# Kernel optimization log

Hardware: AMD Instinct MI355X
Metric: run time of the kernel (lower is better)

Reference implementation:

```python
import jax, jax.numpy as jnp
import numpy as np

D_MODEL, D_K, D_V = 512, 64, 64


def setup_inputs() -> dict:
    key = jax.random.key(0)
    ks = jax.random.split(key, 9)
    b, n = 8, 4096
    scale = 1.0 / np.sqrt(D_MODEL)
    return {
        "q": jax.random.normal(ks[0], (b, n, D_MODEL), jnp.float32),
        "k": jax.random.normal(ks[1], (b, n, D_MODEL), jnp.float32),
        "v": jax.random.normal(ks[2], (b, n, D_MODEL), jnp.float32),
        "Wq": jax.random.normal(ks[3], (D_MODEL, D_K), jnp.float32) * scale,
        "bq": jnp.zeros((D_K,), jnp.float32),
        "Wk": jax.random.normal(ks[4], (D_MODEL, D_K), jnp.float32) * scale,
        "bk": jnp.zeros((D_K,), jnp.float32),
        "Wv": jax.random.normal(ks[5], (D_MODEL, D_V), jnp.float32) * scale,
        "bv": jnp.zeros((D_V,), jnp.float32),
        "mask": 0,
    }


def reference(q, k, v, Wq, bq, Wk, bk, Wv, bv, mask):
    # linear projections (torch Linear: x @ W^T + b; here W stored as [in,out])
    qp = jnp.einsum("bnd,de->bne", q, Wq) + bq  # (b,n,d_k)
    kp = jnp.einsum("bnd,de->bne", k, Wk) + bk  # (b,n,d_k)
    vp = jnp.einsum("bnd,de->bne", v, Wv) + bv  # (b,n,d_v)
    temper = D_K ** 0.5
    attn = jnp.einsum("bqe,bke->bqk", qp, kp) / temper  # (b,n,n)
    # original: attn[attn == mask] = -inf (equality mask on scores)
    attn = jnp.where(attn == jnp.float32(mask), -jnp.inf, attn)
    # NOTE: original's `attn.masked_fill(look_ahead_mask==0, -inf)` is NOT
    # in-place and its result is discarded, so look_ahead_mask has no effect.
    attn = jax.nn.softmax(attn, axis=-1)
    return jnp.einsum("bqk,bkv->bqv", attn, vp)  # (b,n,d_v)
```

## Files before the change

### kernel.cpp

```cpp
#include <hip/hip_runtime.h>

typedef _Float16 f16;
typedef _Float16 f16x2 __attribute__((ext_vector_type(2)));
typedef _Float16 f16x4 __attribute__((ext_vector_type(4)));
typedef _Float16 f16x8 __attribute__((ext_vector_type(8)));
typedef __fp16   h16x2 __attribute__((ext_vector_type(2)));
typedef float    f32x4 __attribute__((ext_vector_type(4)));
typedef float    f32x16 __attribute__((ext_vector_type(16)));

static constexpr float L2E = 1.44269504088896340736f;
static constexpr float QSC = 0.18033688011112042f;

static __device__ __forceinline__ f32x4 mfma16(f16x8 a, f16x8 b, f32x4 c) {
    return __builtin_amdgcn_mfma_f32_16x16x32_f16(a, b, c, 0, 0, 0);
}
static __device__ __forceinline__ f32x16 mfma32(f16x8 a, f16x8 b, f32x16 c) {
    return __builtin_amdgcn_mfma_f32_32x32x16_f16(a, b, c, 0, 0, 0);
}
static __device__ __forceinline__ f16x2 cvt_pk(float a, float b) {
    h16x2 t = __builtin_amdgcn_cvt_pkrtz(a, b);
    return __builtin_bit_cast(f16x2, t);
}
static __device__ __forceinline__ void gload16(const void* g, void* l) {
    __builtin_amdgcn_global_load_lds(
        (const __attribute__((address_space(1))) unsigned int*)g,
        (__attribute__((address_space(3))) unsigned int*)l, 16, 0, 0);
}

__global__ void ah_wt_prep(const float* __restrict__ Wq,
                           const float* __restrict__ Wk,
                           const float* __restrict__ Wv,
                           f16* __restrict__ WT) {
    const float* W = (blockIdx.x == 0) ? Wq : (blockIdx.x == 1) ? Wk : Wv;
    f16* o = WT + (size_t)blockIdx.x * (64 * 512);
    for (int i = threadIdx.x; i < 64 * 512; i += blockDim.x) {
        int col = i >> 9, e = i & 511;
        o[i] = (f16)W[e * 64 + col];
    }
}

__global__ __launch_bounds__(256) void ah_proj(
    const float* __restrict__ Xq, const float* __restrict__ Xk, const float* __restrict__ Xv,
    const float* __restrict__ bq, const float* __restrict__ bk, const float* __restrict__ bv,
    const f16* __restrict__ WT,
    f16* __restrict__ qp, f16* __restrict__ kp, f16* __restrict__ vpT) {

    const int tens = blockIdx.y;
    const float* X    = (tens == 0) ? Xq : (tens == 1) ? Xk : Xv;
    const float* bias = (tens == 0) ? bq : (tens == 1) ? bk : bv;
    const f16* wt = WT + (size_t)tens * (64 * 512);
    const float osc = (tens == 0) ? QSC : 1.0f;

    const int lane = threadIdx.x & 63;
    const int wave = threadIdx.x >> 6;
    const int l15 = lane & 15, g = lane >> 4;
    const int row0 = blockIdx.x * 128;
    const int wrow = wave * 32;

    f32x4 acc[2][4];
#pragma unroll
    for (int a = 0; a < 2; ++a)
#pragma unroll
        for (int b = 0; b < 4; ++b) acc[a][b] = (f32x4){0.f, 0.f, 0.f, 0.f};

#pragma unroll 4
    for (int ec = 0; ec < 16; ++ec) {
        f16x8 af[2];
#pragma unroll
        for (int rf = 0; rf < 2; ++rf) {
            const float* px = X + (size_t)(row0 + wrow + rf * 16 + l15) * 512 + ec * 32 + g * 8;
            float4 v0 = *(const float4*)px;
            float4 v1 = *(const float4*)(px + 4);
            f16x2 p0 = cvt_pk(v0.x, v0.y);
            f16x2 p1 = cvt_pk(v0.z, v0.w);
            f16x2 p2 = cvt_pk(v1.x, v1.y);
            f16x2 p3 = cvt_pk(v1.z, v1.w);
            f16x8 a;
            a[0] = p0[0]; a[1] = p0[1]; a[2] = p1[0]; a[3] = p1[1];
            a[4] = p2[0]; a[5] = p2[1]; a[6] = p3[0]; a[7] = p3[1];
            af[rf] = a;
        }
#pragma unroll
        for (int cf = 0; cf < 4; ++cf) {
            f16x8 bfr = *(const f16x8*)(wt + (size_t)(cf * 16 + l15) * 512 + ec * 32 + g * 8);
#pragma unroll
            for (int rf = 0; rf < 2; ++rf)
                acc[rf][cf] = mfma16(af[rf], bfr, acc[rf][cf]);
        }
    }

    __shared__ __align__(16) f16 lds[128 * 68];
#pragma unroll
    for (int rf = 0; rf < 2; ++rf)
#pragma unroll
        for (int cf = 0; cf < 4; ++cf) {
            float b = bias[cf * 16 + l15];
#pragma unroll
            for (int r = 0; r < 4; ++r) {
                int rr = wrow + rf * 16 + g * 4 + r;
                lds[rr * 68 + cf * 16 + l15] = (f16)((acc[rf][cf][r] + b) * osc);
            }
        }
    __syncthreads();

    if (tens < 2) {
        f16* o = ((tens == 0) ? qp : kp) + (size_t)row0 * 64;
        for (int c = threadIdx.x; c < 128 * 16; c += 256) {
            int r = c >> 4, ch = c & 15;
            *(f16x4*)(o + r * 64 + ch * 4) = *(const f16x4*)(&lds[r * 68 + ch * 4]);
        }
    } else {
        int b = row0 >> 12, n0 = row0 & 4095;
        f16* o = vpT + (size_t)b * 64 * 4096 + n0;
        for (int c = threadIdx.x; c < 64 * 32; c += 256) {
            int d = c >> 5, nch = c & 31;
            f16x4 v;
#pragma unroll
            for (int j = 0; j < 4; ++j) v[j] = lds[(nch * 4 + j) * 68 + d];
            *(f16x4*)(o + (size_t)d * 4096 + nch * 4) = v;
        }
    }
}

__global__ __launch_bounds__(512, 2) void ah_attn(
    const f16* __restrict__ qp, const f16* __restrict__ kp, const f16* __restrict__ vpT,
    const int* __restrict__ maskp, float* __restrict__ out) {

    const int id = blockIdx.x;
    const int batch = id & 7, qtile = id >> 3;
    const int lane = threadIdx.x & 63, wave = threadIdx.x >> 6;
    const int l31 = lane & 31, hi2 = lane >> 5;
    const int s = wave & 3, qg = wave >> 2;
    const int q0 = qtile * 128 + qg * 64;
    const float mthr = L2E * (float)maskp[0];

    const f16* qpb = qp + (size_t)batch * 4096 * 64;
    const f16* kpb = kp + (size_t)batch * 4096 * 64;
    const f16* vpb = vpT + (size_t)batch * 64 * 4096;

    __shared__ __align__(16) char smem[65536];
    __shared__ float mlx[2][4][2][32];

    const int krow = lane >> 3;
    const int vrow = lane >> 2;
    const int eswzK = (lane & 7) ^ krow;
    const int eswzV = (lane & 3) ^ (vrow & 3);
    const int swzK = l31 & 7, swzV = l31 & 3;

#define STAGE(DB, IT) do {                                                          \
    const int _k0 = (((IT) * 4 + s) << 5);                                          \
    char* _b = smem + ((s * 2 + (DB)) * 8192) + (qg ? 4096 : 0);                    \
    if (qg == 0) {                                                                  \
        _Pragma("unroll")                                                           \
        for (int _j = 0; _j < 4; ++_j)                                              \
            gload16(kpb + (size_t)(_k0 + _j * 8 + krow) * 64 + eswzK * 8,           \
                    _b + _j * 1024);                                                \
    } else {                                                                        \
        _Pragma("unroll")                                                           \
        for (int _j = 0; _j < 4; ++_j)                                              \
            gload16(vpb + (size_t)(_j * 16 + vrow) * 4096 + _k0 + eswzV * 8,        \
                    _b + _j * 1024);                                                \
    }                                                                               \
} while (0)

    f16x8 qf_[2][4];
#pragma unroll
    for (int qt = 0; qt < 2; ++qt)
#pragma unroll
        for (int st = 0; st < 4; ++st)
            qf_[qt][st] = *(const f16x8*)(qpb + (size_t)(q0 + qt * 32 + l31) * 64 + st * 16 + hi2 * 8);

    f32x16 oacc[2][2];
#pragma unroll
    for (int dt = 0; dt < 2; ++dt)
#pragma unroll
        for (int qt = 0; qt < 2; ++qt)
#pragma unroll
            for (int r = 0; r < 16; ++r) oacc[dt][qt][r] = 0.f;
    float ps[2] = {0.f, 0.f};

    STAGE(0, 0);
    int db = 0;
    for (int it = 0; it < 32; ++it) {
        if (it < 31) {
            STAGE(db ^ 1, it + 1);
            asm volatile("s_waitcnt vmcnt(4)" ::: "memory");
        } else {
            asm volatile("s_waitcnt vmcnt(0)" ::: "memory");
        }
        __builtin_amdgcn_s_barrier();
        __builtin_amdgcn_sched_barrier(0);

        const char* kb = smem + (s * 2 + db) * 8192;
        const char* vb = kb + 4096;

        f16x8 ka[4];
#pragma unroll
        for (int st = 0; st < 4; ++st)
            ka[st] = *(const f16x8*)(kb + l31 * 128 + (((st * 2 + hi2) ^ swzK) << 4));
        f32x16 sacc[2];
#pragma unroll
        for (int qt = 0; qt < 2; ++qt)
#pragma unroll
            for (int r = 0; r < 16; ++r) sacc[qt][r] = 0.f;
#pragma unroll
        for (int st = 0; st < 4; ++st)
#pragma unroll
            for (int qt = 0; qt < 2; ++qt)
                sacc[qt] = mfma32(ka[st], qf_[qt][st], sacc[qt]);

        f16x8 av[2][2];
#pragma unroll
        for (int dt = 0; dt < 2; ++dt)
#pragma unroll
            for (int t = 0; t < 2; ++t) {
                const char* p = vb + (dt * 32 + l31) * 64 + hi2 * 8;
                *(f16x4*)(&av[dt][t])       = *(const f16x4*)(p + (((t * 2 + 0) ^ swzV) << 4));
                *((f16x4*)(&av[dt][t]) + 1) = *(const f16x4*)(p + (((t * 2 + 1) ^ swzV) << 4));
            }

        f16x8 pb_[2][2];
#pragma unroll
        for (int qt = 0; qt < 2; ++qt)
#pragma unroll
            for (int t = 0; t < 2; ++t)
#pragma unroll
                for (int w = 0; w < 4; ++w) {
                    float s0 = sacc[qt][t * 8 + 2 * w];
                    float s1 = sacc[qt][t * 8 + 2 * w + 1];
                    float e0 = __builtin_amdgcn_exp2f(s0);
                    float e1 = __builtin_amdgcn_exp2f(s1);
                    float p0 = (s0 == mthr) ? 0.f : e0;
                    float p1 = (s1 == mthr) ? 0.f : e1;
                    ps[qt] += p0 + p1;
                    ((f16x2*)(&pb_[qt][t]))[w] = cvt_pk(p0, p1);
                }

#pragma unroll
        for (int dt = 0; dt < 2; ++dt)
#pragma unroll
            for (int qt = 0; qt < 2; ++qt)
#pragma unroll
                for (int t = 0; t < 2; ++t)
                    oacc[dt][qt] = mfma32(av[dt][t], pb_[qt][t], oacc[dt][qt]);

        __builtin_amdgcn_sched_barrier(0);
        __builtin_amdgcn_s_barrier();
        __builtin_amdgcn_sched_barrier(0);
        db ^= 1;
    }
#undef STAGE

    ps[0] += __shfl_xor(ps[0], 32);
    ps[1] += __shfl_xor(ps[1], 32);
    if (lane < 32) { mlx[qg][s][0][lane] = ps[0]; mlx[qg][s][1][lane] = ps[1]; }
    __syncthreads();

    float* SC = (float*)smem;
#define SCI(B, DT, QT, R) ((((qg * 2 + (B)) * 64) + ((DT) * 2 + (QT)) * 16 + (R)) * 64 + lane)
    if (s >= 2) {
#pragma unroll
        for (int dt = 0; dt < 2; ++dt)
#pragma unroll
            for (int qt = 0; qt < 2; ++qt)
#pragma unroll
                for (int r = 0; r < 16; ++r)
                    SC[SCI(s - 2, dt, qt, r)] = oacc[dt][qt][r];
    }
    __syncthreads();
    if (s < 2) {
#pragma unroll
        for (int dt = 0; dt < 2; ++dt)
#pragma unroll
            for (int qt = 0; qt < 2; ++qt)
#pragma unroll
                for (int r = 0; r < 16; ++r)
                    oacc[dt][qt][r] += SC[SCI(s, dt, qt, r)];
        if (s == 1) {
#pragma unroll
            for (int dt = 0; dt < 2; ++dt)
#pragma unroll
                for (int qt = 0; qt < 2; ++qt)
#pragma unroll
                    for (int r = 0; r < 16; ++r)
                        SC[SCI(1, dt, qt, r)] = oacc[dt][qt][r];
        }
    }
    __syncthreads();
    if (s == 0) {
        float inv[2];
#pragma unroll
        for (int qt = 0; qt < 2; ++qt)
            inv[qt] = 1.0f / (mlx[qg][0][qt][l31] + mlx[qg][1][qt][l31] +
                              mlx[qg][2][qt][l31] + mlx[qg][3][qt][l31]);
#pragma unroll
        for (int qt = 0; qt < 2; ++qt) {
            float* o0 = out + ((size_t)batch * 4096 + q0 + qt * 32 + l31) * 64;
#pragma unroll
            for (int dt = 0; dt < 2; ++dt)
#pragma unroll
                for (int rg = 0; rg < 4; ++rg) {
                    float4 v;
                    v.x = (oacc[dt][qt][rg * 4 + 0] + SC[SCI(1, dt, qt, rg * 4 + 0)]) * inv[qt];
                    v.y = (oacc[dt][qt][rg * 4 + 1] + SC[SCI(1, dt, qt, rg * 4 + 1)]) * inv[qt];
                    v.z = (oacc[dt][qt][rg * 4 + 2] + SC[SCI(1, dt, qt, rg * 4 + 2)]) * inv[qt];
                    v.w = (oacc[dt][qt][rg * 4 + 3] + SC[SCI(1, dt, qt, rg * 4 + 3)]) * inv[qt];
                    *(float4*)(o0 + dt * 32 + rg * 8 + hi2 * 4) = v;
                }
        }
    }
#undef SCI
}

extern "C" void kernel_launch(void* const* d_in, const int* in_sizes, int n_in,
                              void* d_out, int out_size, void* d_ws, size_t ws_size,
                              hipStream_t stream) {
    const float* q  = (const float*)d_in[0];
    const float* k  = (const float*)d_in[1];
    const float* v  = (const float*)d_in[2];
    const float* Wq = (const float*)d_in[3];
    const float* bq = (const float*)d_in[4];
    const float* Wk = (const float*)d_in[5];
    const float* bk = (const float*)d_in[6];
    const float* Wv = (const float*)d_in[7];
    const float* bv = (const float*)d_in[8];
    const int* mask = (const int*)d_in[9];
    float* out = (float*)d_out;

    const size_t NTOK = (size_t)8 * 4096;
    f16* qp  = (f16*)d_ws;
    f16* kp  = qp + NTOK * 64;
    f16* vpT = kp + NTOK * 64;
    f16* WT  = vpT + NTOK * 64;

    ah_wt_prep<<<dim3(3), 256, 0, stream>>>(Wq, Wk, Wv, WT);
    ah_proj<<<dim3(256, 3), 256, 0, stream>>>(q, k, v, bq, bk, bv, WT, qp, kp, vpT);
    ah_attn<<<dim3(256), 512, 0, stream>>>(qp, kp, vpT, mask, out);
}
```

Baseline: 130.4 us.

## Double-buffer projection loads through LDS with async global_load_lds and smaller tiles

Rewrites the projection kernel to stage X and W tiles into swizzled, double-buffered LDS using direct global-to-LDS loads, so the next K-chunk is prefetched while the current one is computed. The tile shrinks from 128 to 64 rows per block, which doubles the grid and adds an occupancy hint in the launch bounds. This targets the latency-bound direct global loads of the fp32 inputs in the projection stage. It costs 48KB of LDS per block and adds a barrier on every chunk.

```diff
diff --git a/kernel.cpp b/kernel.cpp
--- a/kernel.cpp
+++ b/kernel.cpp
@@ -39,7 +39,7 @@
     }
 }
 
-__global__ __launch_bounds__(256) void ah_proj(
+__global__ __launch_bounds__(256, 3) void ah_proj(
     const float* __restrict__ Xq, const float* __restrict__ Xk, const float* __restrict__ Xv,
     const float* __restrict__ bq, const float* __restrict__ bk, const float* __restrict__ bv,
     const f16* __restrict__ WT,
@@ -54,66 +54,100 @@
     const int lane = threadIdx.x & 63;
     const int wave = threadIdx.x >> 6;
     const int l15 = lane & 15, g = lane >> 4;
-    const int row0 = blockIdx.x * 128;
-    const int wrow = wave * 32;
-
-    f32x4 acc[2][4];
-#pragma unroll
-    for (int a = 0; a < 2; ++a)
-#pragma unroll
-        for (int b = 0; b < 4; ++b) acc[a][b] = (f32x4){0.f, 0.f, 0.f, 0.f};
-
-#pragma unroll 4
-    for (int ec = 0; ec < 16; ++ec) {
-        f16x8 af[2];
-#pragma unroll
-        for (int rf = 0; rf < 2; ++rf) {
-            const float* px = X + (size_t)(row0 + wrow + rf * 16 + l15) * 512 + ec * 32 + g * 8;
-            float4 v0 = *(const float4*)px;
-            float4 v1 = *(const float4*)(px + 4);
-            f16x2 p0 = cvt_pk(v0.x, v0.y);
-            f16x2 p1 = cvt_pk(v0.z, v0.w);
-            f16x2 p2 = cvt_pk(v1.x, v1.y);
-            f16x2 p3 = cvt_pk(v1.z, v1.w);
+    const int row0 = blockIdx.x * 64;
+    const int wrow = wave * 16;
+
+    __shared__ __align__(16) char smem[49152];
+
+    const int rswz = l15 & 7;
+
+#define PSTAGE(DB, KC) do {                                                           \
+    char* _xb = smem + (DB) * 24576;                                                  \
+    char* _wb = _xb + 16384;                                                          \
+    _Pragma("unroll")                                                                 \
+    for (int _j = 0; _j < 4; ++_j) {                                                  \
+        int _lr = wave * 16 + _j * 4 + (lane >> 4);                  \
+        int _su = (lane & 15) ^ (_lr & 7);                           \
+        gload16(X + (size_t)(row0 + _lr) * 512 + (KC) * 64 + _su * 4,                 \
+                _xb + (wave * 16 + _j * 4) * 256);                                    \
+    }                                                                                 \
+    _Pragma("unroll")                                                                 \
+    for (int _j = 0; _j < 2; ++_j) {                                                  \
+        int _lr = wave * 16 + _j * 8 + (lane >> 3);               \
+        int _su = (lane & 7) ^ (_lr & 7);                                             \
+        gload16(wt + (size_t)_lr * 512 + (KC) * 64 + _su * 8,                         \
+                _wb + (wave * 16 + _j * 8) * 128);                                    \
+    }                                                                                 \
+} while (0)
+
+    f32x4 acc[4];
+#pragma unroll
+    for (int b = 0; b < 4; ++b) acc[b] = (f32x4){0.f, 0.f, 0.f, 0.f};
+
+    PSTAGE(0, 0);
+    int db = 0;
+    for (int kc = 0; kc < 8; ++kc) {
+        if (kc < 7) {
+            PSTAGE(db ^ 1, kc + 1);
+            asm volatile("s_waitcnt vmcnt(6)" ::: "memory");
+        } else {
+            asm volatile("s_waitcnt vmcnt(0)" ::: "memory");
+        }
+        __builtin_amdgcn_s_barrier();
+        __builtin_amdgcn_sched_barrier(0);
+
+        const char* xb = smem + db * 24576;
+        const char* wb = xb + 16384;
+
+#pragma unroll
+        for (int sub = 0; sub < 2; ++sub) {
+            const char* xr = xb + (wrow + l15) * 256;
+            int u0 = sub * 8 + g * 2;
+            float4 v0 = *(const float4*)(xr + ((u0 ^ rswz) << 4));
+            float4 v1 = *(const float4*)(xr + (((u0 + 1) ^ rswz) << 4));
             f16x8 a;
+            f16x2 p0 = cvt_pk(v0.x, v0.y), p1 = cvt_pk(v0.z, v0.w);
+            f16x2 p2 = cvt_pk(v1.x, v1.y), p3 = cvt_pk(v1.z, v1.w);
             a[0] = p0[0]; a[1] = p0[1]; a[2] = p1[0]; a[3] = p1[1];
             a[4] = p2[0]; a[5] = p2[1]; a[6] = p3[0]; a[7] = p3[1];
-            af[rf] = a;
-        }
-#pragma unroll
-        for (int cf = 0; cf < 4; ++cf) {
-            f16x8 bfr = *(const f16x8*)(wt + (size_t)(cf * 16 + l15) * 512 + ec * 32 + g * 8);
-#pragma unroll
-            for (int rf = 0; rf < 2; ++rf)
-                acc[rf][cf] = mfma16(af[rf], bfr, acc[rf][cf]);
-        }
-    }
-
-    __shared__ __align__(16) f16 lds[128 * 68];
-#pragma unroll
-    for (int rf = 0; rf < 2; ++rf)
-#pragma unroll
-        for (int cf = 0; cf < 4; ++cf) {
-            float b = bias[cf * 16 + l15];
-#pragma unroll
-            for (int r = 0; r < 4; ++r) {
-                int rr = wrow + rf * 16 + g * 4 + r;
-                lds[rr * 68 + cf * 16 + l15] = (f16)((acc[rf][cf][r] + b) * osc);
+#pragma unroll
+            for (int cf = 0; cf < 4; ++cf) {
+                f16x8 bfr = *(const f16x8*)(wb + (cf * 16 + l15) * 128 +
+                                            (((sub * 4 + g) ^ rswz) << 4));
+                acc[cf] = mfma16(a, bfr, acc[cf]);
             }
         }
+
+        __builtin_amdgcn_sched_barrier(0);
+        __builtin_amdgcn_s_barrier();
+        __builtin_amdgcn_sched_barrier(0);
+        db ^= 1;
+    }
+#undef PSTAGE
+
+    f16* lds = (f16*)smem;
+#pragma unroll
+    for (int cf = 0; cf < 4; ++cf) {
+        float b = bias[cf * 16 + l15];
+#pragma unroll
+        for (int r = 0; r < 4; ++r) {
+            int rr = wrow + g * 4 + r;
+            lds[rr * 68 + cf * 16 + l15] = (f16)((acc[cf][r] + b) * osc);
+        }
+    }
     __syncthreads();
 
     if (tens < 2) {
         f16* o = ((tens == 0) ? qp : kp) + (size_t)row0 * 64;
-        for (int c = threadIdx.x; c < 128 * 16; c += 256) {
+        for (int c = threadIdx.x; c < 64 * 16; c += 256) {
             int r = c >> 4, ch = c & 15;
             *(f16x4*)(o + r * 64 + ch * 4) = *(const f16x4*)(&lds[r * 68 + ch * 4]);
         }
     } else {
         int b = row0 >> 12, n0 = row0 & 4095;
         f16* o = vpT + (size_t)b * 64 * 4096 + n0;
-        for (int c = threadIdx.x; c < 64 * 32; c += 256) {
-            int d = c >> 5, nch = c & 31;
+        for (int c = threadIdx.x; c < 64 * 16; c += 256) {
+            int d = c >> 4, nch = c & 15;
             f16x4 v;
 #pragma unroll
             for (int j = 0; j < 4; ++j) v[j] = lds[(nch * 4 + j) * 68 + d];
@@ -334,6 +368,6 @@
     f16* WT  = vpT + NTOK * 64;
 
     ah_wt_prep<<<dim3(3), 256, 0, stream>>>(Wq, Wk, Wv, WT);
-    ah_proj<<<dim3(256, 3), 256, 0, stream>>>(q, k, v, bq, bk, bv, WT, qp, kp, vpT);
+    ah_proj<<<dim3(512, 3), 256, 0, stream>>>(q, k, v, bq, bk, bv, WT, qp, kp, vpT);
     ah_attn<<<dim3(256), 512, 0, stream>>>(qp, kp, vpT, mask, out);
 }
```

Result: faster. 116.2 us (-10.9%).

## Stage projection weights in LDS and halve rows per block in ah_proj

Applied to the files above, without the earlier changes.

The projection kernel now copies the 64x512 fp16 weight slice into padded LDS once per block and reads B fragments from LDS rather than global memory. Each block covers 64 rows instead of 128 (one 16-row fragment per wave), and the grid doubles to 512x3 with a launch-bounds hint of 2 blocks per CU. The aim is to cut repeated global weight loads and expose more parallelism for the memory-bound fp32 input reads. In exchange, each block pays a 64KB weight copy and an extra barrier, and the large LDS allocation may limit occupancy.

```diff
diff --git a/kernel.cpp b/kernel.cpp
--- a/kernel.cpp
+++ b/kernel.cpp
@@ -39,7 +39,7 @@
     }
 }
 
-__global__ __launch_bounds__(256) void ah_proj(
+__global__ __launch_bounds__(256, 2) void ah_proj(
     const float* __restrict__ Xq, const float* __restrict__ Xk, const float* __restrict__ Xv,
     const float* __restrict__ bq, const float* __restrict__ bk, const float* __restrict__ bv,
     const f16* __restrict__ WT,
@@ -54,66 +54,69 @@
     const int lane = threadIdx.x & 63;
     const int wave = threadIdx.x >> 6;
     const int l15 = lane & 15, g = lane >> 4;
-    const int row0 = blockIdx.x * 128;
-    const int wrow = wave * 32;
-
-    f32x4 acc[2][4];
-#pragma unroll
-    for (int a = 0; a < 2; ++a)
-#pragma unroll
-        for (int b = 0; b < 4; ++b) acc[a][b] = (f32x4){0.f, 0.f, 0.f, 0.f};
+    const int row0 = blockIdx.x * 64;
+
+    __shared__ __align__(16) f16 wlds[64 * 520];
+
+    {
+        int t = threadIdx.x;
+        int row = t >> 2, q = t & 3;
+        const f16* src = wt + (size_t)row * 512 + q * 128;
+        f16* dst = &wlds[row * 520 + q * 128];
+#pragma unroll
+        for (int i = 0; i < 16; ++i)
+            *(f16x8*)(dst + i * 8) = *(const f16x8*)(src + i * 8);
+    }
+    __syncthreads();
+
+    f32x4 acc[4];
+#pragma unroll
+    for (int b = 0; b < 4; ++b) acc[b] = (f32x4){0.f, 0.f, 0.f, 0.f};
+
+    const float* xrow = X + (size_t)(row0 + wave * 16 + l15) * 512;
 
 #pragma unroll 4
     for (int ec = 0; ec < 16; ++ec) {
-        f16x8 af[2];
-#pragma unroll
-        for (int rf = 0; rf < 2; ++rf) {
-            const float* px = X + (size_t)(row0 + wrow + rf * 16 + l15) * 512 + ec * 32 + g * 8;
-            float4 v0 = *(const float4*)px;
-            float4 v1 = *(const float4*)(px + 4);
-            f16x2 p0 = cvt_pk(v0.x, v0.y);
-            f16x2 p1 = cvt_pk(v0.z, v0.w);
-            f16x2 p2 = cvt_pk(v1.x, v1.y);
-            f16x2 p3 = cvt_pk(v1.z, v1.w);
-            f16x8 a;
-            a[0] = p0[0]; a[1] = p0[1]; a[2] = p1[0]; a[3] = p1[1];
-            a[4] = p2[0]; a[5] = p2[1]; a[6] = p3[0]; a[7] = p3[1];
-            af[rf] = a;
-        }
+        const float* px = xrow + ec * 32 + g * 8;
+        float4 v0 = *(const float4*)px;
+        float4 v1 = *(const float4*)(px + 4);
+        f16x2 p0 = cvt_pk(v0.x, v0.y), p1 = cvt_pk(v0.z, v0.w);
+        f16x2 p2 = cvt_pk(v1.x, v1.y), p3 = cvt_pk(v1.z, v1.w);
+        f16x8 a;
+        a[0] = p0[0]; a[1] = p0[1]; a[2] = p1[0]; a[3] = p1[1];
+        a[4] = p2[0]; a[5] = p2[1]; a[6] = p3[0]; a[7] = p3[1];
 #pragma unroll
         for (int cf = 0; cf < 4; ++cf) {
-            f16x8 bfr = *(const f16x8*)(wt + (size_t)(cf * 16 + l15) * 512 + ec * 32 + g * 8);
-#pragma unroll
-            for (int rf = 0; rf < 2; ++rf)
-                acc[rf][cf] = mfma16(af[rf], bfr, acc[rf][cf]);
-        }
-    }
-
-    __shared__ __align__(16) f16 lds[128 * 68];
-#pragma unroll
-    for (int rf = 0; rf < 2; ++rf)
-#pragma unroll
-        for (int cf = 0; cf < 4; ++cf) {
-            float b = bias[cf * 16 + l15];
-#pragma unroll
-            for (int r = 0; r < 4; ++r) {
-                int rr = wrow + rf * 16 + g * 4 + r;
-                lds[rr * 68 + cf * 16 + l15] = (f16)((acc[rf][cf][r] + b) * osc);
-            }
-        }
+            f16x8 bfr = *(const f16x8*)(&wlds[(cf * 16 + l15) * 520 + (ec * 4 + g) * 8]);
+            acc[cf] = mfma16(a, bfr, acc[cf]);
+        }
+    }
+
+    __syncthreads();
+
+    f16* lds = wlds;
+#pragma unroll
+    for (int cf = 0; cf < 4; ++cf) {
+        float b = bias[cf * 16 + l15];
+#pragma unroll
+        for (int r = 0; r < 4; ++r) {
+            int rr = wave * 16 + g * 4 + r;
+            lds[rr * 68 + cf * 16 + l15] = (f16)((acc[cf][r] + b) * osc);
+        }
+    }
     __syncthreads();
 
     if (tens < 2) {
         f16* o = ((tens == 0) ? qp : kp) + (size_t)row0 * 64;
-        for (int c = threadIdx.x; c < 128 * 16; c += 256) {
+        for (int c = threadIdx.x; c < 64 * 16; c += 256) {
             int r = c >> 4, ch = c & 15;
             *(f16x4*)(o + r * 64 + ch * 4) = *(const f16x4*)(&lds[r * 68 + ch * 4]);
         }
     } else {
         int b = row0 >> 12, n0 = row0 & 4095;
         f16* o = vpT + (size_t)b * 64 * 4096 + n0;
-        for (int c = threadIdx.x; c < 64 * 32; c += 256) {
-            int d = c >> 5, nch = c & 31;
+        for (int c = threadIdx.x; c < 64 * 16; c += 256) {
+            int d = c >> 4, nch = c & 15;
             f16x4 v;
 #pragma unroll
             for (int j = 0; j < 4; ++j) v[j] = lds[(nch * 4 + j) * 68 + d];
@@ -334,6 +337,6 @@
     f16* WT  = vpT + NTOK * 64;
 
     ah_wt_prep<<<dim3(3), 256, 0, stream>>>(Wq, Wk, Wv, WT);
-    ah_proj<<<dim3(256, 3), 256, 0, stream>>>(q, k, v, bq, bk, bv, WT, qp, kp, vpT);
+    ah_proj<<<dim3(512, 3), 256, 0, stream>>>(q, k, v, bq, bk, bv, WT, qp, kp, vpT);
     ah_attn<<<dim3(256), 512, 0, stream>>>(qp, kp, vpT, mask, out);
 }
```

Result: faster. 127.1 us (-2.5%).

## Double-buffer projection operands through LDS via async loads and raise MFMA priority

Applied to the files above, without the earlier changes.

The projection kernel now stages X and weight tiles into a double-buffered LDS area using direct global-to-LDS loads with an XOR swizzle. The next chunk is prefetched while the current one is computed, instead of each wave issuing synchronous global loads per iteration. Launch bounds now request 4 blocks per CU. The attention loop also raises wave priority around its MFMA blocks. In exchange, the projection path adds barriers and 40KB of shared memory per block, which may limit occupancy.

```diff
diff --git a/kernel.cpp b/kernel.cpp
--- a/kernel.cpp
+++ b/kernel.cpp
@@ -39,7 +39,7 @@
     }
 }
 
-__global__ __launch_bounds__(256) void ah_proj(
+__global__ __launch_bounds__(256, 4) void ah_proj(
     const float* __restrict__ Xq, const float* __restrict__ Xk, const float* __restrict__ Xv,
     const float* __restrict__ bq, const float* __restrict__ bk, const float* __restrict__ bv,
     const f16* __restrict__ WT,
@@ -57,39 +57,74 @@
     const int row0 = blockIdx.x * 128;
     const int wrow = wave * 32;
 
+    __shared__ __align__(16) char smem[40960];
+
+    const int xr8 = lane >> 3;
+    const int xsu = (lane & 7) ^ (xr8 & 7);
+
+#define PSTAGE(KC) do {                                                              \
+    char* _xb = smem + ((KC) & 1) * 20480;                                           \
+    char* _wb = _xb + 16384;                                                         \
+    _Pragma("unroll")                                                                \
+    for (int _j = 0; _j < 4; ++_j)                                                   \
+        gload16(X + (size_t)(row0 + wrow + _j * 8 + xr8) * 512 + (KC) * 32 + xsu * 4,\
+                _xb + (wrow + _j * 8) * 128);                                        \
+    gload16(wt + (size_t)(wave * 16 + (lane >> 2)) * 512 + (KC) * 32 + (lane & 3) * 8,\
+            _wb + wave * 1024);                                                      \
+} while (0)
+
     f32x4 acc[2][4];
 #pragma unroll
     for (int a = 0; a < 2; ++a)
 #pragma unroll
         for (int b = 0; b < 4; ++b) acc[a][b] = (f32x4){0.f, 0.f, 0.f, 0.f};
 
-#pragma unroll 4
-    for (int ec = 0; ec < 16; ++ec) {
-        f16x8 af[2];
-#pragma unroll
-        for (int rf = 0; rf < 2; ++rf) {
-            const float* px = X + (size_t)(row0 + wrow + rf * 16 + l15) * 512 + ec * 32 + g * 8;
-            float4 v0 = *(const float4*)px;
-            float4 v1 = *(const float4*)(px + 4);
-            f16x2 p0 = cvt_pk(v0.x, v0.y);
-            f16x2 p1 = cvt_pk(v0.z, v0.w);
-            f16x2 p2 = cvt_pk(v1.x, v1.y);
-            f16x2 p3 = cvt_pk(v1.z, v1.w);
-            f16x8 a;
-            a[0] = p0[0]; a[1] = p0[1]; a[2] = p1[0]; a[3] = p1[1];
-            a[4] = p2[0]; a[5] = p2[1]; a[6] = p3[0]; a[7] = p3[1];
-            af[rf] = a;
-        }
-#pragma unroll
-        for (int cf = 0; cf < 4; ++cf) {
-            f16x8 bfr = *(const f16x8*)(wt + (size_t)(cf * 16 + l15) * 512 + ec * 32 + g * 8);
-#pragma unroll
-            for (int rf = 0; rf < 2; ++rf)
-                acc[rf][cf] = mfma16(af[rf], bfr, acc[rf][cf]);
-        }
-    }
-
-    __shared__ __align__(16) f16 lds[128 * 68];
+#define PCOMP(KC) do {                                                               \
+    const char* _xb = smem + ((KC) & 1) * 20480;                                     \
+    const char* _wb = _xb + 16384;                                                   \
+    f16x8 af[2];                                                                     \
+    _Pragma("unroll")                                                                \
+    for (int rf = 0; rf < 2; ++rf) {                                                 \
+        const char* cb = _xb + (wrow + rf * 16 + l15) * 128;                         \
+        float4 v0 = *(const float4*)(cb + (((2 * g + 0) ^ (l15 & 7)) << 4));         \
+        float4 v1 = *(const float4*)(cb + (((2 * g + 1) ^ (l15 & 7)) << 4));         \
+        f16x2 p0 = cvt_pk(v0.x, v0.y), p1 = cvt_pk(v0.z, v0.w);                      \
+        f16x2 p2 = cvt_pk(v1.x, v1.y), p3 = cvt_pk(v1.z, v1.w);                      \
+        f16x8 a;                                                                     \
+        a[0] = p0[0]; a[1] = p0[1]; a[2] = p1[0]; a[3] = p1[1];                      \
+        a[4] = p2[0]; a[5] = p2[1]; a[6] = p3[0]; a[7] = p3[1];                      \
+        af[rf] = a;                                                                  \
+    }                                                                                \
+    _Pragma("unroll")                                                                \
+    for (int cf = 0; cf < 4; ++cf) {                                                 \
+        f16x8 bfr = *(const f16x8*)(_wb + (cf * 16 + l15) * 64 + g * 16);            \
+        _Pragma("unroll")                                                            \
+        for (int rf = 0; rf < 2; ++rf)                                               \
+            acc[rf][cf] = mfma16(af[rf], bfr, acc[rf][cf]);                          \
+    }                                                                                \
+} while (0)
+
+    PSTAGE(0);
+    for (int kc = 0; kc < 16; ++kc) {
+        if (kc < 15) {
+            PSTAGE(kc + 1);
+            asm volatile("s_waitcnt vmcnt(5)" ::: "memory");
+        } else {
+            asm volatile("s_waitcnt vmcnt(0)" ::: "memory");
+        }
+        __builtin_amdgcn_sched_barrier(0);
+        __builtin_amdgcn_s_barrier();
+        __builtin_amdgcn_sched_barrier(0);
+        PCOMP(kc);
+        __builtin_amdgcn_sched_barrier(0);
+        __builtin_amdgcn_s_barrier();
+        __builtin_amdgcn_sched_barrier(0);
+    }
+#undef PSTAGE
+#undef PCOMP
+    __syncthreads();
+
+    f16* lds = (f16*)smem;
 #pragma unroll
     for (int rf = 0; rf < 2; ++rf)
 #pragma unroll
@@ -203,11 +238,13 @@
         for (int qt = 0; qt < 2; ++qt)
 #pragma unroll
             for (int r = 0; r < 16; ++r) sacc[qt][r] = 0.f;
+        __builtin_amdgcn_s_setprio(1);
 #pragma unroll
         for (int st = 0; st < 4; ++st)
 #pragma unroll
             for (int qt = 0; qt < 2; ++qt)
                 sacc[qt] = mfma32(ka[st], qf_[qt][st], sacc[qt]);
+        __builtin_amdgcn_s_setprio(0);
 
         f16x8 av[2][2];
 #pragma unroll
@@ -236,6 +273,7 @@
                     ((f16x2*)(&pb_[qt][t]))[w] = cvt_pk(p0, p1);
                 }
 
+        __builtin_amdgcn_s_setprio(1);
 #pragma unroll
         for (int dt = 0; dt < 2; ++dt)
 #pragma unroll
@@ -243,6 +281,7 @@
 #pragma unroll
                 for (int t = 0; t < 2; ++t)
                     oacc[dt][qt] = mfma32(av[dt][t], pb_[qt][t], oacc[dt][qt]);
+        __builtin_amdgcn_s_setprio(0);
 
         __builtin_amdgcn_sched_barrier(0);
         __builtin_amdgcn_s_barrier();
```

Result: faster. 122.2 us (-6.3%).
